# Kernel tuning notes

Hardware: AMD Instinct MI355X
Metric: run time of the kernel (lower is better)

## Reference

```python
import jax, jax.numpy as jnp
import numpy as np

# B=batch, T=time, H=hidden_size, D=vocos_dim, I=intermediate_dim, L=num_layers,
# CB=codebook_size, CD=codebook_dim (factorized VQ)
B, T, H, D, I, L, CB, CD = 8, 2048, 1024, 384, 2048, 12, 8192, 8


def _ln(h, g, b, eps=1e-6):
    # torch LayerNorm over last dim (biased variance)
    m = h.mean(-1, keepdims=True)
    v = h.var(-1, keepdims=True)
    return (h - m) / jnp.sqrt(v + eps) * g + b


def _conv1d(x, w, b, groups=1):
    # x: (B, Cin, T), w: (Cout, Cin//groups, 7), same-pad k=7
    y = jax.lax.conv_general_dilated(
        x, w, window_strides=(1,), padding=[(3, 3)],
        dimension_numbers=('NCH', 'OIH', 'NCH'), feature_group_count=groups)
    return y + b[None, :, None]


def setup_inputs() -> dict:
    key = jax.random.key(0)
    ks = iter(jax.random.split(key, 32))
    def nrm(shape):
        return jax.random.normal(next(ks), shape, jnp.float32) * 0.02
    d = {}
    d['x'] = jax.random.normal(next(ks), (B, T, H), jnp.float32)
    # VocosBackbone (encoder): embed conv + LN + 12 ConvNeXt blocks + final LN
    d['enc_embed_w'] = nrm((D, H, 7)); d['enc_embed_b'] = jnp.zeros((D,), jnp.float32)
    d['enc_norm_g'] = jnp.ones((D,), jnp.float32); d['enc_norm_b'] = jnp.zeros((D,), jnp.float32)
    d['enc_dw_w'] = nrm((L, D, 1, 7)); d['enc_dw_b'] = jnp.zeros((L, D), jnp.float32)
    d['enc_ln_g'] = jnp.ones((L, D), jnp.float32); d['enc_ln_b'] = jnp.zeros((L, D), jnp.float32)
    d['enc_w1'] = nrm((L, I, D)); d['enc_b1'] = jnp.zeros((L, I), jnp.float32)
    d['enc_w2'] = nrm((L, D, I)); d['enc_b2'] = jnp.zeros((L, D), jnp.float32)
    d['enc_gamma'] = jnp.full((L, D), 1.0 / L, jnp.float32)  # layer_scale init 1/num_layers
    d['enc_fnorm_g'] = jnp.ones((D,), jnp.float32); d['enc_fnorm_b'] = jnp.zeros((D,), jnp.float32)
    # nn.Linear(vocos_dim, hidden_size)
    d['enc_out_w'] = nrm((H, D)); d['enc_out_b'] = jnp.zeros((H,), jnp.float32)
    # Factorized ResidualVQ (single quantizer): 1024 -> 8, 8192-entry codebook, 8 -> 1024
    d['vq_in_w'] = nrm((CD, H)); d['vq_in_b'] = jnp.zeros((CD,), jnp.float32)
    d['codebook'] = jax.random.normal(next(ks), (CB, CD), jnp.float32)
    d['vq_out_w'] = nrm((H, CD)); d['vq_out_b'] = jnp.zeros((H,), jnp.float32)
    return d


def _encode(x, ew, eb, ng, nb, dww, dwb, lng, lnb, w1, b1, w2, b2, gamma, fg, fb, ow, ob):
    # x: (B, T, H) -> encoder output (B, T, H)
    h = _conv1d(x.transpose(0, 2, 1), ew, eb)            # (B, D, T)
    h = _ln(h.transpose(0, 2, 1), ng, nb)                # (B, T, D)
    for i in range(L):
        res = h
        y = _conv1d(h.transpose(0, 2, 1), dww[i], dwb[i], groups=D)  # depthwise (B, D, T)
        y = _ln(y.transpose(0, 2, 1), lng[i], lnb[i])                # (B, T, D)
        y = jax.nn.gelu(y @ w1[i].T + b1[i], approximate=False)       # (B, T, I)
        y = (y @ w2[i].T + b2[i]) * gamma[i]                          # (B, T, D)
        h = res + y
    h = _ln(h, fg, fb)
    return h @ ow.T + ob                                  # (B, T, H)


def _quantize(enc, in_w, in_b, codebook, out_w, out_b):
    z_e = enc @ in_w.T + in_b                             # (B, T, CD)
    z_n = z_e / jnp.maximum(jnp.linalg.norm(z_e, axis=-1, keepdims=True), 1e-12)
    cb_n = codebook / jnp.maximum(jnp.linalg.norm(codebook, axis=-1, keepdims=True), 1e-12)
    sim = jnp.einsum('btd,nd->btn', z_n, cb_n)            # cosine sim == argmin l2 on normalized vecs
    idx = jnp.argmax(sim, axis=-1)                        # (B, T) int
    z_q = codebook[idx]                                   # (B, T, CD) unnormalized codebook entries
    z_q = z_e + jax.lax.stop_gradient(z_q - z_e)          # straight-through estimator
    quantized = z_q @ out_w.T + out_b                     # (B, T, H)
    return idx, quantized


def reference(x, enc_embed_w, enc_embed_b, enc_norm_g, enc_norm_b, enc_dw_w, enc_dw_b,
              enc_ln_g, enc_ln_b, enc_w1, enc_b1, enc_w2, enc_b2, enc_gamma,
              enc_fnorm_g, enc_fnorm_b, enc_out_w, enc_out_b,
              vq_in_w, vq_in_b, codebook, vq_out_w, vq_out_b):
    enc = _encode(x, enc_embed_w, enc_embed_b, enc_norm_g, enc_norm_b, enc_dw_w, enc_dw_b,
                  enc_ln_g, enc_ln_b, enc_w1, enc_b1, enc_w2, enc_b2, enc_gamma,
                  enc_fnorm_g, enc_fnorm_b, enc_out_w, enc_out_b)
    idx, quantized = _quantize(enc, vq_in_w, vq_in_b, codebook, vq_out_w, vq_out_b)
    # RepCodec.quantize returns (indices (B,T), quantized_out.transpose(1,2) -> (B,T,H))
    return idx, quantized
```

## Files before the change

kernel.cpp:

```cpp
#include <hip/hip_runtime.h>
#include <math.h>


typedef _Float16 h8_t __attribute__((ext_vector_type(8)));
typedef _Float16 h4_t __attribute__((ext_vector_type(4)));
typedef float f4_t __attribute__((ext_vector_type(4)));

__device__ __forceinline__ float gelu_exact(float x){
  return 0.5f * x * (1.0f + erff(x * 0.70710678118654752f));
}

__device__ __forceinline__ void split4(const float4& a, h4_t& hi, h4_t& lo){
  float f[4] = {a.x,a.y,a.z,a.w};
  #pragma unroll
  for (int t=0;t<4;t++){
    _Float16 hh = (_Float16)f[t];
    hi[t] = hh;
    lo[t] = (_Float16)(f[t] - (float)hh);
  }
}

__device__ __forceinline__ int swz(int row, int kg){
  return row*32 + ((kg ^ ((row>>1)&3))<<3);
}

__device__ __forceinline__ void xcd_remap(int& bx, int& by){
  const int gx = gridDim.x;
  const int nwg = gx * gridDim.y;
  int bid = by*gx + bx;
  if ((nwg & 7) == 0){
    bid = (bid & 7)*(nwg >> 3) + (bid >> 3);
    bx = bid % gx; by = bid / gx;
  }
}


__global__ __launch_bounds__(256) void prep_wk_split(const float* __restrict__ w,
                                                     _Float16* __restrict__ wh,
                                                     _Float16* __restrict__ wl){
  int i = blockIdx.x*256 + threadIdx.x;
  if (i >= 384*1024) return;
  int d = i >> 10, c = i & 1023;
  #pragma unroll
  for (int k=0;k<7;k++){
    float v = w[(size_t)d*(1024*7) + (size_t)c*7 + k];
    _Float16 hh = (_Float16)v;
    wh[(size_t)k*393216 + i] = hh;
    wl[(size_t)k*393216 + i] = (_Float16)(v - (float)hh);
  }
}

__global__ __launch_bounds__(256) void prep_cb(const float* __restrict__ cb, float* __restrict__ cbn){
  int e = blockIdx.x*256 + threadIdx.x;
  if (e >= 8192) return;
  float v[8], s = 0.f;
  #pragma unroll
  for (int cd=0; cd<8; ++cd){ v[cd] = cb[(size_t)e*8+cd]; s += v[cd]*v[cd]; }
  float inv = 1.0f / fmaxf(sqrtf(s), 1e-12f);
  #pragma unroll
  for (int cd=0; cd<8; ++cd) cbn[(size_t)e*8+cd] = v[cd]*inv;
}

__global__ __launch_bounds__(256) void split_pair(const float* __restrict__ a, const float* __restrict__ b,
                                                  _Float16* __restrict__ ah, _Float16* __restrict__ al,
                                                  _Float16* __restrict__ bh, _Float16* __restrict__ bl,
                                                  int n4){
  int i = blockIdx.x*256 + threadIdx.x;
  if (i >= n4) return;
  h4_t hi, lo;
  float4 va = ((const float4*)a)[i];
  split4(va, hi, lo);
  ((h4_t*)ah)[i] = hi; ((h4_t*)al)[i] = lo;
  float4 vb = ((const float4*)b)[i];
  split4(vb, hi, lo);
  ((h4_t*)bh)[i] = hi; ((h4_t*)bl)[i] = lo;
}

__global__ __launch_bounds__(256) void split_one(const float* __restrict__ a,
                                                 _Float16* __restrict__ ah, _Float16* __restrict__ al,
                                                 int n4){
  int i = blockIdx.x*256 + threadIdx.x;
  if (i >= n4) return;
  h4_t hi, lo;
  float4 va = ((const float4*)a)[i];
  split4(va, hi, lo);
  ((h4_t*)ah)[i] = hi; ((h4_t*)al)[i] = lo;
}

template<int BN, int EPI>
__global__ __launch_bounds__(256,2) void gemm_s(
    const _Float16* __restrict__ Ah, const _Float16* __restrict__ Al, int lda,
    const _Float16* __restrict__ Bh, const _Float16* __restrict__ Bl, int ldb,
    const float* __restrict__ bias, const float* __restrict__ gamma,
    float* __restrict__ C, _Float16* __restrict__ Ch, _Float16* __restrict__ Cl,
    int ldc, int K)
{
  constexpr int NF = BN/32;
  __shared__ _Float16 AsH[4096], AsL[4096];
  __shared__ _Float16 BsH[BN*32], BsL[BN*32];
  const int tid = threadIdx.x;
  int bx = blockIdx.x, by = blockIdx.y;
  xcd_remap(bx, by);
  const int m0 = by*128, n0 = bx*BN;
  const int srow = tid>>2, kgs = tid&3, koff = kgs*8;
  const _Float16* pAh = Ah + (size_t)(m0+srow)*lda + koff;
  const _Float16* pAl = Al + (size_t)(m0+srow)*lda + koff;
  const _Float16* pBh = Bh + (size_t)(n0+srow)*ldb + koff;
  const _Float16* pBl = Bl + (size_t)(n0+srow)*ldb + koff;
  const int sA0 = swz(srow, kgs), sA1 = swz(srow+64, kgs);
  const int lane = tid & 63, wid = tid >> 6;
  const int wm = (wid>>1)*64, wn = (wid&1)*(BN/2);
  const int fr = lane & 15, kg = lane >> 4;
  f4_t acc[4][NF] = {};
  h8_t rah0 = *(const h8_t*)(pAh);
  h8_t rah1 = *(const h8_t*)(pAh + (size_t)64*lda);
  h8_t ral0 = *(const h8_t*)(pAl);
  h8_t ral1 = *(const h8_t*)(pAl + (size_t)64*lda);
  h8_t rbh0 = *(const h8_t*)(pBh);
  h8_t rbl0 = *(const h8_t*)(pBl);
  h8_t rbh1, rbl1;
  if constexpr (BN == 128){
    rbh1 = *(const h8_t*)(pBh + (size_t)64*ldb);
    rbl1 = *(const h8_t*)(pBl + (size_t)64*ldb);
  }
  for (int k0 = 0; k0 < K; k0 += 32){
    __syncthreads();
    *(h8_t*)(AsH + sA0) = rah0; *(h8_t*)(AsL + sA0) = ral0;
    *(h8_t*)(AsH + sA1) = rah1; *(h8_t*)(AsL + sA1) = ral1;
    *(h8_t*)(BsH + sA0) = rbh0; *(h8_t*)(BsL + sA0) = rbl0;
    if constexpr (BN == 128){
      *(h8_t*)(BsH + sA1) = rbh1; *(h8_t*)(BsL + sA1) = rbl1;
    }
    if (k0 + 32 < K){
      const int kn = k0 + 32;
      rah0 = *(const h8_t*)(pAh + kn);
      rah1 = *(const h8_t*)(pAh + (size_t)64*lda + kn);
      ral0 = *(const h8_t*)(pAl + kn);
      ral1 = *(const h8_t*)(pAl + (size_t)64*lda + kn);
      rbh0 = *(const h8_t*)(pBh + kn);
      rbl0 = *(const h8_t*)(pBl + kn);
      if constexpr (BN == 128){
        rbh1 = *(const h8_t*)(pBh + (size_t)64*ldb + kn);
        rbl1 = *(const h8_t*)(pBl + (size_t)64*ldb + kn);
      }
    }
    __syncthreads();
    h8_t ah[4], al[4], bh[NF], bl[NF];
    #pragma unroll
    for (int m=0;m<4;m++){
      int o = swz(wm + fr + m*16, kg);
      ah[m] = *(const h8_t*)(AsH + o);
      al[m] = *(const h8_t*)(AsL + o);
    }
    #pragma unroll
    for (int n=0;n<NF;n++){
      int o = swz(wn + fr + n*16, kg);
      bh[n] = *(const h8_t*)(BsH + o);
      bl[n] = *(const h8_t*)(BsL + o);
    }
    #pragma unroll
    for (int m=0;m<4;m++)
      #pragma unroll
      for (int n=0;n<NF;n++){
        acc[m][n] = __builtin_amdgcn_mfma_f32_16x16x32_f16(al[m], bh[n], acc[m][n], 0,0,0);
        acc[m][n] = __builtin_amdgcn_mfma_f32_16x16x32_f16(ah[m], bl[n], acc[m][n], 0,0,0);
        acc[m][n] = __builtin_amdgcn_mfma_f32_16x16x32_f16(ah[m], bh[n], acc[m][n], 0,0,0);
      }
  }
  float bj[NF], gj[NF];
  #pragma unroll
  for (int n=0;n<NF;n++){
    int col = n0 + wn + n*16 + fr;
    bj[n] = bias ? bias[col] : 0.0f;
    gj[n] = (EPI==2) ? gamma[col] : 0.0f;
  }
  #pragma unroll
  for (int m=0;m<4;m++){
    #pragma unroll
    for (int r=0;r<4;r++){
      const int row = m0 + wm + m*16 + kg*4 + r;
      #pragma unroll
      for (int n=0;n<NF;n++){
        const int col = n0 + wn + n*16 + fr;
        float v = acc[m][n][r] + bj[n];
        if (EPI==0){
          C[(size_t)row*ldc + col] = v;
        } else if (EPI==1){
          v = gelu_exact(v);
          _Float16 hh = (_Float16)v;
          Ch[(size_t)row*ldc + col] = hh;
          Cl[(size_t)row*ldc + col] = (_Float16)(v - (float)hh);
        } else if (EPI==2){
          C[(size_t)row*ldc + col] += gj[n]*v;
        } else {
          _Float16 hh = (_Float16)v;
          Ch[(size_t)row*ldc + col] = hh;
          Cl[(size_t)row*ldc + col] = (_Float16)(v - (float)hh);
        }
      }
    }
  }
}

template<int EPI>
__global__ __launch_bounds__(512,2) void gemm_t(
    const _Float16* __restrict__ Ah, const _Float16* __restrict__ Al, int lda,
    const _Float16* __restrict__ Bh, const _Float16* __restrict__ Bl, int ldb,
    const float* __restrict__ bias,
    _Float16* __restrict__ Ch, _Float16* __restrict__ Cl,
    int ldc, int K)
{
  __shared__ _Float16 AsH[8192], AsL[8192], BsH[4096], BsL[4096];
  const int tid = threadIdx.x;
  int bx = blockIdx.x, by = blockIdx.y;
  xcd_remap(bx, by);
  const int m0 = by*256, n0 = bx*128;
  const int srow = tid>>2, kgs = tid&3, koff = kgs*8;
  const _Float16* pAh = Ah + (size_t)(m0+srow)*lda + koff;
  const _Float16* pAl = Al + (size_t)(m0+srow)*lda + koff;
  const _Float16* pBh = Bh + (size_t)(n0+srow)*ldb + koff;
  const _Float16* pBl = Bl + (size_t)(n0+srow)*ldb + koff;
  const int sA0 = swz(srow, kgs), sA1 = swz(srow+128, kgs);
  const int lane = tid & 63, wid = tid >> 6;
  const int wm = (wid>>1)*64, wn = (wid&1)*64;
  const int fr = lane & 15, kg = lane >> 4;
  f4_t acc[4][4] = {};
  h8_t rah0 = *(const h8_t*)(pAh);
  h8_t rah1 = *(const h8_t*)(pAh + (size_t)128*lda);
  h8_t ral0 = *(const h8_t*)(pAl);
  h8_t ral1 = *(const h8_t*)(pAl + (size_t)128*lda);
  h8_t rbh0 = *(const h8_t*)(pBh);
  h8_t rbl0 = *(const h8_t*)(pBl);
  for (int k0 = 0; k0 < K; k0 += 32){
    __syncthreads();
    *(h8_t*)(AsH + sA0) = rah0; *(h8_t*)(AsL + sA0) = ral0;
    *(h8_t*)(AsH + sA1) = rah1; *(h8_t*)(AsL + sA1) = ral1;
    *(h8_t*)(BsH + sA0) = rbh0; *(h8_t*)(BsL + sA0) = rbl0;
    if (k0 + 32 < K){
      const int kn = k0 + 32;
      rah0 = *(const h8_t*)(pAh + kn);
      rah1 = *(const h8_t*)(pAh + (size_t)128*lda + kn);
      ral0 = *(const h8_t*)(pAl + kn);
      ral1 = *(const h8_t*)(pAl + (size_t)128*lda + kn);
      rbh0 = *(const h8_t*)(pBh + kn);
      rbl0 = *(const h8_t*)(pBl + kn);
    }
    __syncthreads();
    h8_t ah[4], al[4], bh[4], bl[4];
    #pragma unroll
    for (int m=0;m<4;m++){
      int o = swz(wm + fr + m*16, kg);
      ah[m] = *(const h8_t*)(AsH + o);
      al[m] = *(const h8_t*)(AsL + o);
    }
    #pragma unroll
    for (int n=0;n<4;n++){
      int o = swz(wn + fr + n*16, kg);
      bh[n] = *(const h8_t*)(BsH + o);
      bl[n] = *(const h8_t*)(BsL + o);
    }
    #pragma unroll
    for (int m=0;m<4;m++)
      #pragma unroll
      for (int n=0;n<4;n++){
        acc[m][n] = __builtin_amdgcn_mfma_f32_16x16x32_f16(al[m], bh[n], acc[m][n], 0,0,0);
        acc[m][n] = __builtin_amdgcn_mfma_f32_16x16x32_f16(ah[m], bl[n], acc[m][n], 0,0,0);
        acc[m][n] = __builtin_amdgcn_mfma_f32_16x16x32_f16(ah[m], bh[n], acc[m][n], 0,0,0);
      }
  }
  float bj[4];
  #pragma unroll
  for (int n=0;n<4;n++){
    int col = n0 + wn + n*16 + fr;
    bj[n] = bias ? bias[col] : 0.0f;
  }
  #pragma unroll
  for (int m=0;m<4;m++){
    #pragma unroll
    for (int r=0;r<4;r++){
      const int row = m0 + wm + m*16 + kg*4 + r;
      #pragma unroll
      for (int n=0;n<4;n++){
        const int col = n0 + wn + n*16 + fr;
        float v = acc[m][n][r] + bj[n];
        if (EPI==1) v = gelu_exact(v);
        _Float16 hh = (_Float16)v;
        Ch[(size_t)row*ldc + col] = hh;
        Cl[(size_t)row*ldc + col] = (_Float16)(v - (float)hh);
      }
    }
  }
}

__global__ __launch_bounds__(256,2) void embed_f16(
    const _Float16* __restrict__ xh, const _Float16* __restrict__ xl,
    const _Float16* __restrict__ wkh, const _Float16* __restrict__ wkl,
    const float* __restrict__ bias, float* __restrict__ C)
{
  __shared__ _Float16 AsH[4096], AsL[4096], BsH[2048], BsL[2048];
  const int tid = threadIdx.x;
  int bx = blockIdx.x, by = blockIdx.y;
  xcd_remap(bx, by);
  const int m0 = by*128, n0 = bx*64;
  const int srow = tid>>2, kgs = tid&3, koff = kgs*8;
  const int sA0 = swz(srow, kgs), sA1 = swz(srow+64, kgs);
  const int lane = tid & 63, wid = tid >> 6;
  const int wm = (wid>>1)*64, wn = (wid&1)*32;
  const int fr = lane & 15, kg = lane >> 4;
  const int r0 = m0 + srow, r1 = r0 + 64;
  const int t0 = r0 & 2047, t1 = r1 & 2047;
  f4_t acc[4][2] = {};
  const h8_t zero8 = {0,0,0,0,0,0,0,0};
  h8_t rah0, rah1, ral0, ral1, rbh0, rbl0;
  auto load_tile = [&](int kt, h8_t& a0, h8_t& a1, h8_t& l0, h8_t& l1, h8_t& bh, h8_t& bl){
    const int k = kt >> 5;
    const int k0 = (kt & 31) << 5;
    const bool v0 = (unsigned)(t0 + k - 3) < 2048u;
    const bool v1 = (unsigned)(t1 + k - 3) < 2048u;
    a0 = zero8; a1 = zero8; l0 = zero8; l1 = zero8;
    if (v0){
      const size_t o = (size_t)(r0 + k - 3)*1024 + k0 + koff;
      a0 = *(const h8_t*)(xh + o); l0 = *(const h8_t*)(xl + o);
    }
    if (v1){
      const size_t o = (size_t)(r1 + k - 3)*1024 + k0 + koff;
      a1 = *(const h8_t*)(xh + o); l1 = *(const h8_t*)(xl + o);
    }
    const size_t wo = (size_t)k*393216 + (size_t)(n0+srow)*1024 + k0 + koff;
    bh = *(const h8_t*)(wkh + wo); bl = *(const h8_t*)(wkl + wo);
  };
  load_tile(0, rah0, rah1, ral0, ral1, rbh0, rbl0);
  for (int kt = 0; kt < 224; ++kt){
    __syncthreads();
    *(h8_t*)(AsH+sA0) = rah0; *(h8_t*)(AsL+sA0) = ral0;
    *(h8_t*)(AsH+sA1) = rah1; *(h8_t*)(AsL+sA1) = ral1;
    *(h8_t*)(BsH+sA0) = rbh0; *(h8_t*)(BsL+sA0) = rbl0;
    if (kt + 1 < 224)
      load_tile(kt+1, rah0, rah1, ral0, ral1, rbh0, rbl0);
    __syncthreads();
    h8_t ah[4], al[4], bh[2], bl[2];
    #pragma unroll
    for (int m=0;m<4;m++){
      int o = swz(wm + fr + m*16, kg);
      ah[m] = *(const h8_t*)(AsH + o);
      al[m] = *(const h8_t*)(AsL + o);
    }
    #pragma unroll
    for (int n=0;n<2;n++){
      int o = swz(wn + fr + n*16, kg);
      bh[n] = *(const h8_t*)(BsH + o);
      bl[n] = *(const h8_t*)(BsL + o);
    }
    #pragma unroll
    for (int m=0;m<4;m++)
      #pragma unroll
      for (int n=0;n<2;n++){
        acc[m][n] = __builtin_amdgcn_mfma_f32_16x16x32_f16(al[m], bh[n], acc[m][n], 0,0,0);
        acc[m][n] = __builtin_amdgcn_mfma_f32_16x16x32_f16(ah[m], bl[n], acc[m][n], 0,0,0);
        acc[m][n] = __builtin_amdgcn_mfma_f32_16x16x32_f16(ah[m], bh[n], acc[m][n], 0,0,0);
      }
  }
  #pragma unroll
  for (int m=0;m<4;m++){
    #pragma unroll
    for (int r=0;r<4;r++){
      const int row = m0 + wm + m*16 + kg*4 + r;
      #pragma unroll
      for (int n=0;n<2;n++){
        const int col = n0 + wn + n*16 + fr;
        C[(size_t)row*384 + col] = acc[m][n][r] + bias[col];
      }
    }
  }
}

template<bool CONV, bool SPLIT>
__global__ __launch_bounds__(384) void ln_kernel(
    const float* __restrict__ in,
    const float* __restrict__ dw, const float* __restrict__ db,
    const float* __restrict__ g, const float* __restrict__ b,
    float* __restrict__ out, _Float16* __restrict__ oh, _Float16* __restrict__ ol)
{
  __shared__ float rs[6], rs2[6], stat[2];
  const int m = blockIdx.x, d = threadIdx.x;
  float v;
  if (CONV){
    const int t = m & 2047;
    float a = db[d];
    #pragma unroll
    for (int k=0;k<7;k++){
      int tt = t + k - 3;
      if ((unsigned)tt < 2048u) a = fmaf(in[(size_t)(m + k - 3)*384 + d], dw[d*7 + k], a);
    }
    v = a;
  } else {
    v = in[(size_t)m*384 + d];
  }
  float s = v, s2 = v*v;
  #pragma unroll
  for (int o=1;o<64;o<<=1){ s += __shfl_xor(s,o); s2 += __shfl_xor(s2,o); }
  const int wid = d >> 6, lane = d & 63;
  if (lane == 0){ rs[wid]=s; rs2[wid]=s2; }
  __syncthreads();
  if (d == 0){
    float S=0.f, S2=0.f;
    #pragma unroll
    for (int w=0;w<6;w++){ S+=rs[w]; S2+=rs2[w]; }
    float mean = S*(1.0f/384.0f);
    float var = fmaxf(S2*(1.0f/384.0f) - mean*mean, 0.0f);
    stat[0]=mean; stat[1]=1.0f/sqrtf(var + 1e-6f);
  }
  __syncthreads();
  float o = (v - stat[0])*stat[1]*g[d] + b[d];
  if (SPLIT){
    _Float16 hh = (_Float16)o;
    oh[(size_t)m*384 + d] = hh;
    ol[(size_t)m*384 + d] = (_Float16)(o - (float)hh);
  } else {
    out[(size_t)m*384 + d] = o;
  }
}


__global__ __launch_bounds__(256) void vq_in_kernel(
    const _Float16* __restrict__ ench, const _Float16* __restrict__ encl,
    const float* __restrict__ wi, const float* __restrict__ bi, float* __restrict__ zn)
{
  __shared__ float sw[8192];
  const int tid = threadIdx.x;
  for (int i = tid*4; i < 8192; i += 1024) *(float4*)&sw[i] = *(const float4*)&wi[i];
  __syncthreads();
  const int wid = tid >> 6, lane = tid & 63;
  const size_t m = (size_t)blockIdx.x*4 + wid;
  float acc[8] = {};
  for (int j=0;j<16;j++){
    float v = (float)ench[m*1024 + j*64 + lane] + (float)encl[m*1024 + j*64 + lane];
    #pragma unroll
    for (int cd=0;cd<8;cd++) acc[cd] = fmaf(v, sw[cd*1024 + j*64 + lane], acc[cd]);
  }
  #pragma unroll
  for (int cd=0;cd<8;cd++)
    #pragma unroll
    for (int o=1;o<64;o<<=1) acc[cd] += __shfl_xor(acc[cd], o);
  if (lane == 0){
    float z[8], s = 0.f;
    #pragma unroll
    for (int cd=0;cd<8;cd++){ z[cd] = acc[cd] + bi[cd]; s += z[cd]*z[cd]; }
    float inv = 1.0f / fmaxf(sqrtf(s), 1e-12f);
    #pragma unroll
    for (int cd=0;cd<8;cd++) zn[m*8+cd] = z[cd]*inv;
  }
}

__global__ __launch_bounds__(256) void vq_argmax(
    const float* __restrict__ zn, const float* __restrict__ cbn,
    int* __restrict__ idx_out, float* __restrict__ idx_f)
{
  __shared__ float sbest[256];
  __shared__ int   sidx[256];
  const int tid = threadIdx.x;
  const int tok = tid & 31, ch = tid >> 5;
  const size_t m = (size_t)blockIdx.x*32 + tok;
  float4 z0 = *(const float4*)&zn[m*8];
  float4 z1 = *(const float4*)&zn[m*8+4];
  float best = -1e30f; int bidx = 0;
  const float* cp = cbn + (size_t)ch*8192;
  #pragma unroll 4
  for (int e = 0; e < 1024; ++e){
    const float4 ca  = *(const float4*)&cp[e*8];
    const float4 cb4 = *(const float4*)&cp[e*8+4];
    float s = z0.x*ca.x + z0.y*ca.y + z0.z*ca.z + z0.w*ca.w
            + z1.x*cb4.x + z1.y*cb4.y + z1.z*cb4.z + z1.w*cb4.w;
    if (s > best){ best = s; bidx = ch*1024 + e; }
  }
  sbest[tid] = best; sidx[tid] = bidx;
  __syncthreads();
  if (tid < 32){
    float b = sbest[tid]; int bi = sidx[tid];
    #pragma unroll
    for (int c=1;c<8;c++){
      float ob = sbest[c*32 + tid];
      if (ob > b){ b = ob; bi = sidx[c*32 + tid]; }
    }
    idx_out[(size_t)blockIdx.x*32 + tid] = bi;
    idx_f [(size_t)blockIdx.x*32 + tid] = (float)bi;
  }
}

__global__ __launch_bounds__(256) void vq_out_kernel(
    const int* __restrict__ idx, const float* __restrict__ cb,
    const float* __restrict__ wo, const float* __restrict__ bo,
    float* __restrict__ outq)
{
  __shared__ float wT[8][1024];
  __shared__ float cbs[16][8];
  __shared__ int idxs[16];
  const int tid = threadIdx.x;
  #pragma unroll
  for (int j=0;j<4;j++){
    int hcol = j*256 + tid;
    float4 w0 = *(const float4*)&wo[(size_t)hcol*8];
    float4 w1 = *(const float4*)&wo[(size_t)hcol*8+4];
    wT[0][hcol]=w0.x; wT[1][hcol]=w0.y; wT[2][hcol]=w0.z; wT[3][hcol]=w0.w;
    wT[4][hcol]=w1.x; wT[5][hcol]=w1.y; wT[6][hcol]=w1.z; wT[7][hcol]=w1.w;
  }
  if (tid < 16) idxs[tid] = idx[blockIdx.x*16 + tid];
  __syncthreads();
  if (tid < 128){ int tk = tid>>3, cd = tid&7; cbs[tk][cd] = cb[(size_t)idxs[tk]*8 + cd]; }
  __syncthreads();
  float bb[4];
  #pragma unroll
  for (int j=0;j<4;j++) bb[j] = bo[j*256+tid];
  for (int tk=0;tk<16;tk++){
    const size_t m = (size_t)blockIdx.x*16 + tk;
    float c0=cbs[tk][0], c1=cbs[tk][1], c2=cbs[tk][2], c3=cbs[tk][3];
    float c4=cbs[tk][4], c5=cbs[tk][5], c6=cbs[tk][6], c7=cbs[tk][7];
    #pragma unroll
    for (int j=0;j<4;j++){
      int hcol = j*256 + tid;
      float v = bb[j];
      v = fmaf(c0, wT[0][hcol], v); v = fmaf(c1, wT[1][hcol], v);
      v = fmaf(c2, wT[2][hcol], v); v = fmaf(c3, wT[3][hcol], v);
      v = fmaf(c4, wT[4][hcol], v); v = fmaf(c5, wT[5][hcol], v);
      v = fmaf(c6, wT[6][hcol], v); v = fmaf(c7, wT[7][hcol], v);
      outq[m*1024 + hcol] = v;
    }
  }
}


extern "C" void kernel_launch(void* const* d_in, const int* in_sizes, int n_in,
                              void* d_out, int out_size, void* d_ws, size_t ws_size,
                              hipStream_t stream) {
  (void)in_sizes; (void)n_in; (void)out_size; (void)ws_size;
  const float* x   = (const float*)d_in[0];
  const float* eww = (const float*)d_in[1];
  const float* ewb = (const float*)d_in[2];
  const float* ng  = (const float*)d_in[3];
  const float* nb  = (const float*)d_in[4];
  const float* dww = (const float*)d_in[5];
  const float* dwb = (const float*)d_in[6];
  const float* lng = (const float*)d_in[7];
  const float* lnb = (const float*)d_in[8];
  const float* w1  = (const float*)d_in[9];
  const float* b1  = (const float*)d_in[10];
  const float* w2  = (const float*)d_in[11];
  const float* b2  = (const float*)d_in[12];
  const float* gma = (const float*)d_in[13];
  const float* fg  = (const float*)d_in[14];
  const float* fb  = (const float*)d_in[15];
  const float* ow  = (const float*)d_in[16];
  const float* ob  = (const float*)d_in[17];
  const float* viw = (const float*)d_in[18];
  const float* vib = (const float*)d_in[19];
  const float* cb  = (const float*)d_in[20];
  const float* vow = (const float*)d_in[21];
  const float* vob = (const float*)d_in[22];
  float* out = (float*)d_out;

  float* ws = (float*)d_ws;
  float* wreg = ws;
  _Float16* wkh = (_Float16*)wreg;
  _Float16* wkl = wkh + 2752512;
  _Float16* w1h = (_Float16*)wreg;
  _Float16* w1l = w1h + 786432;
  _Float16* w2h = w1h + 1572864;
  _Float16* w2l = w1h + 2359296;
  _Float16* owh = (_Float16*)wreg;
  _Float16* owl = owh + 393216;
  float* zn  = wreg + 1048576;
  float* cbn = wreg + 1179648;
  int*  idxb = (int*)(wreg + 1245184);
  float* h   = ws + 2752512;
  float* ylreg = ws + 9043968;
  float* yf32 = ylreg;
  _Float16* ylh = (_Float16*)ylreg;
  _Float16* yll = ylh + 6291456;
  float* y1reg = ws + 15335424;
  _Float16* xh  = (_Float16*)y1reg;
  _Float16* xl  = xh + 16777216;
  _Float16* y1h = (_Float16*)y1reg;
  _Float16* y1l = y1h + 16777216;
  _Float16* ench = y1h;
  _Float16* encl = y1l;

  prep_wk_split<<<dim3(1536), dim3(256), 0, stream>>>(eww, wkh, wkl);
  split_one<<<dim3(16384), dim3(256), 0, stream>>>(x, xh, xl, 4194304);
  embed_f16<<<dim3(6,128), dim3(256), 0, stream>>>(xh, xl, wkh, wkl, ewb, yf32);
  ln_kernel<false,false><<<dim3(16384), dim3(384), 0, stream>>>(
      yf32, nullptr, nullptr, ng, nb, h, nullptr, nullptr);

  for (int i = 0; i < 12; ++i){
    split_pair<<<dim3(768), dim3(256), 0, stream>>>(
        w1 + (size_t)i*786432, w2 + (size_t)i*786432, w1h, w1l, w2h, w2l, 196608);
    ln_kernel<true,true><<<dim3(16384), dim3(384), 0, stream>>>(
        h, dww + (size_t)i*2688, dwb + (size_t)i*384,
        lng + (size_t)i*384, lnb + (size_t)i*384, nullptr, ylh, yll);
    for (int ic = 0; ic < 2; ++ic){
      gemm_t<1><<<dim3(8,64), dim3(512), 0, stream>>>(
          ylh, yll, 384,
          w1h + (size_t)ic*393216, w1l + (size_t)ic*393216, 384,
          b1 + (size_t)i*2048 + (size_t)ic*1024,
          y1h, y1l, 1024, 384);
      gemm_s<64,2><<<dim3(6,128), dim3(256), 0, stream>>>(
          y1h, y1l, 1024,
          w2h + (size_t)ic*1024, w2l + (size_t)ic*1024, 2048,
          (ic == 0) ? (b2 + (size_t)i*384) : nullptr,
          gma + (size_t)i*384,
          h, nullptr, nullptr, 384, 1024);
    }
  }

  ln_kernel<false,true><<<dim3(16384), dim3(384), 0, stream>>>(
      h, nullptr, nullptr, fg, fb, nullptr, ylh, yll);
  split_one<<<dim3(384), dim3(256), 0, stream>>>(ow, owh, owl, 98304);
  gemm_t<3><<<dim3(8,64), dim3(512), 0, stream>>>(
      ylh, yll, 384, owh, owl, 384, ob, ench, encl, 1024, 384);

  prep_cb<<<dim3(32), dim3(256), 0, stream>>>(cb, cbn);
  vq_in_kernel<<<dim3(4096), dim3(256), 0, stream>>>(ench, encl, viw, vib, zn);
  vq_argmax<<<dim3(512), dim3(256), 0, stream>>>(zn, cbn, idxb, out);
  vq_out_kernel<<<dim3(1024), dim3(256), 0, stream>>>(idxb, cb, vow, vob, out + 16384);
}
```

Baseline: 3.732 ms.

## Fold encoder output linear into VQ input projection and tweak GEMM scheduling

```diff
diff --git a/kernel.cpp b/kernel.cpp
--- a/kernel.cpp
+++ b/kernel.cpp
@@ -59,6 +59,25 @@
   float inv = 1.0f / fmaxf(sqrtf(s), 1e-12f);
   #pragma unroll
   for (int cd=0; cd<8; ++cd) cbn[(size_t)e*8+cd] = v[cd]*inv;
+}
+
+__global__ __launch_bounds__(256) void prep_cw(const float* __restrict__ viw, const float* __restrict__ ow,
+                                               const float* __restrict__ vib, const float* __restrict__ ob,
+                                               float* __restrict__ cw, float* __restrict__ cbias){
+  int i = blockIdx.x*256 + threadIdx.x;
+  if (i < 3072){
+    int c = i / 384, d = i - c*384;
+    float acc = 0.f;
+    for (int h=0; h<1024; ++h)
+      acc = fmaf(viw[c*1024+h], ow[(size_t)h*384 + d], acc);
+    cw[i] = acc;
+  }
+  if (blockIdx.x == 0 && threadIdx.x < 8){
+    int c = threadIdx.x;
+    float acc = vib[c];
+    for (int h=0; h<1024; ++h) acc = fmaf(viw[c*1024+h], ob[h], acc);
+    cbias[c] = acc;
+  }
 }
 
 __global__ __launch_bounds__(256) void split_pair(const float* __restrict__ a, const float* __restrict__ b,
@@ -127,9 +146,12 @@
     __syncthreads();
     *(h8_t*)(AsH + sA0) = rah0; *(h8_t*)(AsL + sA0) = ral0;
     *(h8_t*)(AsH + sA1) = rah1; *(h8_t*)(AsL + sA1) = ral1;
-    *(h8_t*)(BsH + sA0) = rbh0; *(h8_t*)(BsL + sA0) = rbl0;
     if constexpr (BN == 128){
+      *(h8_t*)(BsH + sA0) = rbh0; *(h8_t*)(BsL + sA0) = rbl0;
       *(h8_t*)(BsH + sA1) = rbh1; *(h8_t*)(BsL + sA1) = rbl1;
+    } else {
+      if (srow < 64){ *(h8_t*)(BsH + sA0) = rbh0; *(h8_t*)(BsL + sA0) = rbl0; }
+      else          { *(h8_t*)(BsH + sA1 - 2048) = rbh0; *(h8_t*)(BsL + sA1 - 2048) = rbl0; }
     }
     if (k0 + 32 < K){
       const int kn = k0 + 32;
@@ -158,6 +180,7 @@
       bh[n] = *(const h8_t*)(BsH + o);
       bl[n] = *(const h8_t*)(BsL + o);
     }
+    __builtin_amdgcn_s_setprio(1);
     #pragma unroll
     for (int m=0;m<4;m++)
       #pragma unroll
@@ -166,6 +189,7 @@
         acc[m][n] = __builtin_amdgcn_mfma_f32_16x16x32_f16(ah[m], bl[n], acc[m][n], 0,0,0);
         acc[m][n] = __builtin_amdgcn_mfma_f32_16x16x32_f16(ah[m], bh[n], acc[m][n], 0,0,0);
       }
+    __builtin_amdgcn_s_setprio(0);
   }
   float bj[NF], gj[NF];
   #pragma unroll
@@ -312,31 +336,31 @@
   f4_t acc[4][2] = {};
   const h8_t zero8 = {0,0,0,0,0,0,0,0};
   h8_t rah0, rah1, ral0, ral1, rbh0, rbl0;
-  auto load_tile = [&](int kt, h8_t& a0, h8_t& a1, h8_t& l0, h8_t& l1, h8_t& bh, h8_t& bl){
+  auto load_tile = [&](int kt){
     const int k = kt >> 5;
     const int k0 = (kt & 31) << 5;
     const bool v0 = (unsigned)(t0 + k - 3) < 2048u;
     const bool v1 = (unsigned)(t1 + k - 3) < 2048u;
-    a0 = zero8; a1 = zero8; l0 = zero8; l1 = zero8;
+    rah0 = zero8; rah1 = zero8; ral0 = zero8; ral1 = zero8;
     if (v0){
       const size_t o = (size_t)(r0 + k - 3)*1024 + k0 + koff;
-      a0 = *(const h8_t*)(xh + o); l0 = *(const h8_t*)(xl + o);
+      rah0 = *(const h8_t*)(xh + o); ral0 = *(const h8_t*)(xl + o);
     }
     if (v1){
       const size_t o = (size_t)(r1 + k - 3)*1024 + k0 + koff;
-      a1 = *(const h8_t*)(xh + o); l1 = *(const h8_t*)(xl + o);
+      rah1 = *(const h8_t*)(xh + o); ral1 = *(const h8_t*)(xl + o);
     }
     const size_t wo = (size_t)k*393216 + (size_t)(n0+srow)*1024 + k0 + koff;
-    bh = *(const h8_t*)(wkh + wo); bl = *(const h8_t*)(wkl + wo);
+    rbh0 = *(const h8_t*)(wkh + wo); rbl0 = *(const h8_t*)(wkl + wo);
   };
-  load_tile(0, rah0, rah1, ral0, ral1, rbh0, rbl0);
+  load_tile(0);
   for (int kt = 0; kt < 224; ++kt){
     __syncthreads();
     *(h8_t*)(AsH+sA0) = rah0; *(h8_t*)(AsL+sA0) = ral0;
     *(h8_t*)(AsH+sA1) = rah1; *(h8_t*)(AsL+sA1) = ral1;
     *(h8_t*)(BsH+sA0) = rbh0; *(h8_t*)(BsL+sA0) = rbl0;
     if (kt + 1 < 224)
-      load_tile(kt+1, rah0, rah1, ral0, ral1, rbh0, rbl0);
+      load_tile(kt+1);
     __syncthreads();
     h8_t ah[4], al[4], bh[2], bl[2];
     #pragma unroll
@@ -422,21 +446,22 @@
 }
 
 
-__global__ __launch_bounds__(256) void vq_in_kernel(
-    const _Float16* __restrict__ ench, const _Float16* __restrict__ encl,
-    const float* __restrict__ wi, const float* __restrict__ bi, float* __restrict__ zn)
+__global__ __launch_bounds__(256) void vq_ze(
+    const float* __restrict__ y, const float* __restrict__ cw,
+    const float* __restrict__ cbias, float* __restrict__ zn)
 {
-  __shared__ float sw[8192];
+  __shared__ float scw[3072];
   const int tid = threadIdx.x;
-  for (int i = tid*4; i < 8192; i += 1024) *(float4*)&sw[i] = *(const float4*)&wi[i];
+  for (int i = tid; i < 3072; i += 256) scw[i] = cw[i];
   __syncthreads();
   const int wid = tid >> 6, lane = tid & 63;
   const size_t m = (size_t)blockIdx.x*4 + wid;
   float acc[8] = {};
-  for (int j=0;j<16;j++){
-    float v = (float)ench[m*1024 + j*64 + lane] + (float)encl[m*1024 + j*64 + lane];
-    #pragma unroll
-    for (int cd=0;cd<8;cd++) acc[cd] = fmaf(v, sw[cd*1024 + j*64 + lane], acc[cd]);
+  #pragma unroll
+  for (int j=0;j<6;j++){
+    float v = y[m*384 + j*64 + lane];
+    #pragma unroll
+    for (int cd=0;cd<8;cd++) acc[cd] = fmaf(v, scw[cd*384 + j*64 + lane], acc[cd]);
   }
   #pragma unroll
   for (int cd=0;cd<8;cd++)
@@ -445,7 +470,7 @@
   if (lane == 0){
     float z[8], s = 0.f;
     #pragma unroll
-    for (int cd=0;cd<8;cd++){ z[cd] = acc[cd] + bi[cd]; s += z[cd]*z[cd]; }
+    for (int cd=0;cd<8;cd++){ z[cd] = acc[cd] + cbias[cd]; s += z[cd]*z[cd]; }
     float inv = 1.0f / fmaxf(sqrtf(s), 1e-12f);
     #pragma unroll
     for (int cd=0;cd<8;cd++) zn[m*8+cd] = z[cd]*inv;
@@ -566,11 +591,11 @@
   _Float16* w1l = w1h + 786432;
   _Float16* w2h = w1h + 1572864;
   _Float16* w2l = w1h + 2359296;
-  _Float16* owh = (_Float16*)wreg;
-  _Float16* owl = owh + 393216;
   float* zn  = wreg + 1048576;
   float* cbn = wreg + 1179648;
   int*  idxb = (int*)(wreg + 1245184);
+  float* cw  = wreg + 1261568;
+  float* cbias = wreg + 1264640;
   float* h   = ws + 2752512;
   float* ylreg = ws + 9043968;
   float* yf32 = ylreg;
@@ -581,8 +606,6 @@
   _Float16* xl  = xh + 16777216;
   _Float16* y1h = (_Float16*)y1reg;
   _Float16* y1l = y1h + 16777216;
-  _Float16* ench = y1h;
-  _Float16* encl = y1l;
 
   prep_wk_split<<<dim3(1536), dim3(256), 0, stream>>>(eww, wkh, wkl);
   split_one<<<dim3(16384), dim3(256), 0, stream>>>(x, xh, xl, 4194304);
@@ -611,14 +634,11 @@
     }
   }
 
-  ln_kernel<false,true><<<dim3(16384), dim3(384), 0, stream>>>(
-      h, nullptr, nullptr, fg, fb, nullptr, ylh, yll);
-  split_one<<<dim3(384), dim3(256), 0, stream>>>(ow, owh, owl, 98304);
-  gemm_t<3><<<dim3(8,64), dim3(512), 0, stream>>>(
-      ylh, yll, 384, owh, owl, 384, ob, ench, encl, 1024, 384);
-
+  ln_kernel<false,false><<<dim3(16384), dim3(384), 0, stream>>>(
+      h, nullptr, nullptr, fg, fb, yf32, nullptr, nullptr);
+  prep_cw<<<dim3(12), dim3(256), 0, stream>>>(viw, ow, vib, ob, cw, cbias);
   prep_cb<<<dim3(32), dim3(256), 0, stream>>>(cb, cbn);
-  vq_in_kernel<<<dim3(4096), dim3(256), 0, stream>>>(ench, encl, viw, vib, zn);
+  vq_ze<<<dim3(4096), dim3(256), 0, stream>>>(yf32, cw, cbias, zn);
   vq_argmax<<<dim3(512), dim3(256), 0, stream>>>(zn, cbn, idxb, out);
   vq_out_kernel<<<dim3(1024), dim3(256), 0, stream>>>(idxb, cb, vow, vob, out + 16384);
 }
```

Result: no change. 3.752 ms (+0.5%).
